# Performance work log

Hardware: AMD Instinct MI355X
Metric: run time of the kernel (lower is better)

Reference implementation:

```python
import jax, jax.numpy as jnp
import numpy as np

B, TQ, TV = 4, 256, 256
H, D, U = 512, 512, 256  # hidden_size, value_size, units


def setup_inputs() -> dict:
    key = jax.random.key(0)
    ks = jax.random.split(key, 8)
    s = 0.02
    return {
        "query": jax.random.normal(ks[0], (B, TQ, H), dtype=jnp.float32),
        "values": jax.random.normal(ks[1], (B, TV, D), dtype=jnp.float32),
        "W1": jax.random.normal(ks[2], (H, U), dtype=jnp.float32) * s,
        "b1": jnp.zeros((U,), dtype=jnp.float32),
        "W2": jax.random.normal(ks[3], (D, U), dtype=jnp.float32) * s,
        "b2": jnp.zeros((U,), dtype=jnp.float32),
        "V": jax.random.normal(ks[4], (U, 1), dtype=jnp.float32) * s,
        "bV": jnp.zeros((1,), dtype=jnp.float32),
    }


def reference(query, values, W1, b1, W2, b2, V, bV):
    # query: [B,Tq,H]  values: [B,Tv,D]
    q = jnp.einsum("bqh,hu->bqu", query, W1) + b1          # [B,Tq,U]
    v = jnp.einsum("bvd,du->bvu", values, W2) + b2          # [B,Tv,U]
    # tf.repeat over Tq is just a broadcast of v; same math without materializing repeats twice
    hidden = jnp.tanh(q[:, :, None, :] + v[:, None, :, :])  # [B,Tq,Tv,U]
    score = jnp.einsum("bqvu,u->bqv", hidden, V[:, 0]) + bV[0]  # [B,Tq,Tv]
    attn = jax.nn.softmax(score, axis=2)                    # softmax over Tv (axis=2 of score)
    context = jnp.einsum("bqv,bvd->bqd", attn, values)      # [B,Tq,D]
    return context, attn[..., None]                          # weights returned as [B,Tq,Tv,1] like TF
```

## Files before the change

### kernel.cpp

```cpp
#include <hip/hip_runtime.h>
#include <math.h>


typedef float f4 __attribute__((ext_vector_type(4)));
typedef float f2 __attribute__((ext_vector_type(2)));
typedef __attribute__((ext_vector_type(8))) short s8v;
typedef __attribute__((ext_vector_type(4))) unsigned short u4v;
typedef __attribute__((ext_vector_type(8))) unsigned short u8v;

#define B_    4
#define TQ_   256
#define TV_   256
#define D_    512
#define U_    256
#define KDIM  512
#define MROWS 1024

#define C2LOG2E 2.8853900817779268f

#define EVT_U16_OFF   524288
#define ATTN_U16_OFF  786432
#define VALT_U16_OFF 1048576

#if __has_builtin(__builtin_amdgcn_exp2f)
#define EXP2F(x) __builtin_amdgcn_exp2f(x)
#else
#define EXP2F(x) exp2f(x)
#endif
#if __has_builtin(__builtin_amdgcn_rcpf)
#define RCPF(x) __builtin_amdgcn_rcpf(x)
#else
#define RCPF(x) (1.0f / (x))
#endif

__device__ __forceinline__ unsigned short f2bf(float f) {
    union { float f; unsigned u; } v; v.f = f;
    return (unsigned short)((v.u + 0x7FFF + ((v.u >> 16) & 1)) >> 16);
}
__device__ __forceinline__ float bf2f(unsigned short h) {
    union { unsigned u; float f; } v; v.u = (unsigned)h << 16;
    return v.f;
}

__global__ __launch_bounds__(256) void proj_mfma(
    const float* __restrict__ query, const float* __restrict__ values,
    const float* __restrict__ W1, const float* __restrict__ b1,
    const float* __restrict__ W2, const float* __restrict__ b2,
    float* __restrict__ ws)
{
    const int tid = threadIdx.x;
    const int job = blockIdx.y;

    if (job == 2) {
        const int idx = blockIdx.x * 256 + tid;
        const int d   = idx & 511;
        const int vg  = (idx >> 9) & 31;
        const int b   = idx >> 14;
        const float* src = values + ((size_t)b * TV_ + vg * 8) * KDIM + d;
        unsigned short* valT = (unsigned short*)ws + VALT_U16_OFF;
        u8v o;
        #pragma unroll
        for (int j = 0; j < 8; ++j) o[j] = f2bf(src[(size_t)j * KDIM]);
        *(u8v*)(valT + ((size_t)b * D_ + d) * TV_ + vg * 8) = o;
        return;
    }

    __shared__ unsigned short Al[2][32][40];
    __shared__ unsigned short Bl[2][32][40];

    const int proj = job;
    const int x    = blockIdx.x;

    int m0, n0;
    if (proj == 0) { m0 = (x >> 3) * 32; n0 = (x & 7) * 32; }
    else           { m0 = (x & 7) * 32;  n0 = (x >> 3) * 32; }

    const int drow = tid >> 3;
    const int dk   = (tid & 7) * 4;
    const int tcol = drow;
    const int tk   = dk;

    const float* dptr = (proj ? values + (size_t)(n0 + drow) * KDIM
                              : query  + (size_t)(m0 + drow) * KDIM) + dk;
    const float* tptr = (proj ? W2 + (m0 + tcol) : W1 + (n0 + tcol))
                        + (size_t)tk * U_;

    f4 d0;
    float tv0, tv1, tv2, tv3;

#define LOADR(S)                                                        \
    do {                                                                \
        d0 = *(const f4*)(dptr + (size_t)(S) * 32);                     \
        const float* tp = tptr + (size_t)(S) * 32 * U_;                 \
        tv0 = tp[0]; tv1 = tp[U_]; tv2 = tp[2 * U_]; tv3 = tp[3 * U_];  \
    } while (0)

#define WRITEB(BUF)                                                     \
    do {                                                                \
        u4v dd, tt;                                                     \
        dd[0] = f2bf(d0[0]); dd[1] = f2bf(d0[1]);                       \
        dd[2] = f2bf(d0[2]); dd[3] = f2bf(d0[3]);                       \
        tt[0] = f2bf(tv0);   tt[1] = f2bf(tv1);                         \
        tt[2] = f2bf(tv2);   tt[3] = f2bf(tv3);                         \
        unsigned short* ddst = proj ? &Bl[BUF][drow][dk] : &Al[BUF][drow][dk]; \
        unsigned short* tdst = proj ? &Al[BUF][tcol][tk] : &Bl[BUF][tcol][tk]; \
        *(u4v*)ddst = dd;                                               \
        *(u4v*)tdst = tt;                                               \
    } while (0)

    f4 acc = {};

    const int w    = tid >> 6;
    const int l    = tid & 63;
    const int fr   = l & 15;
    const int fk   = (l >> 4) * 8;
    const int band = (w & 1) * 16;
    const int colh = (w >> 1) * 16;

    LOADR(0);
    WRITEB(0);

    for (int s = 0; s < 16; ++s) {
        __syncthreads();
        if (s + 1 < 16) LOADR(s + 1);
        {
            const int bu = s & 1;
            s8v af = *(const s8v*)&Al[bu][band + fr][fk];
            s8v bf = *(const s8v*)&Bl[bu][colh + fr][fk];
            acc = __builtin_amdgcn_mfma_f32_16x16x32_bf16(af, bf, acc, 0, 0, 0);
        }
        if (s + 1 < 16) WRITEB((s + 1) & 1);
    }
#undef LOADR
#undef WRITEB

    const int orow = m0 + band + (l >> 4) * 4;
    const int ocol = n0 + colh + (l & 15);

    if (proj == 0) {
        float* E = ws;
        const float bias = b1[ocol];
        #pragma unroll
        for (int r = 0; r < 4; ++r)
            E[(size_t)(orow + r) * U_ + ocol] =
                EXP2F((acc[r] + bias) * C2LOG2E);
    } else {
        unsigned short* E = (unsigned short*)ws + EVT_U16_OFF;
        #pragma unroll
        for (int r = 0; r < 4; ++r)
            E[(size_t)(orow + r) * MROWS + ocol] =
                f2bf(EXP2F((acc[r] + b2[orow + r]) * C2LOG2E));
    }
}

__global__ __launch_bounds__(256) void score_softmax(
    const float* __restrict__ Vw, float* __restrict__ ws,
    float* __restrict__ out)
{
    __shared__ float redmin[4][2];
    __shared__ float redsum[4][2];

    const int tid = threadIdx.x;
    const int b  = blockIdx.y;
    const int q0 = blockIdx.x * 2;

    const float* eq0 = ws + (size_t)(b * TQ_ + q0) * U_;
    const float* eq1 = eq0 + U_;
    const unsigned short* evp =
        (const unsigned short*)ws + EVT_U16_OFF + (size_t)b * TV_ + tid;
    float* attn = out + (size_t)B_ * TQ_ * D_ + (size_t)(b * TQ_ + q0) * TV_;
    unsigned short* attnbf =
        (unsigned short*)ws + ATTN_U16_OFF + (size_t)(b * TQ_ + q0) * TV_;

    float evA[8], evB[8];
    #pragma unroll
    for (int i = 0; i < 8; ++i) evA[i] = bf2f(evp[(size_t)i * MROWS]);

    f2 p = {0.f, 0.f};
    const f2 one = {1.0f, 1.0f};

#define SGRP(BUF, G)                                                    \
    _Pragma("unroll")                                                   \
    for (int i = 0; i < 8; ++i) {                                       \
        const int u = (G) * 8 + i;                                      \
        f2 eq = {eq0[u], eq1[u]};                      \
        f2 ev2 = {BUF[i], BUF[i]};                                      \
        f2 den = eq * ev2 + one;                      \
        f2 r = {RCPF(den.x), RCPF(den.y)};                              \
        f2 wv = {Vw[u], Vw[u]};                             \
        p = wv * r + p;                               \
    }

    #pragma unroll
    for (int g = 0; g < 32; g += 2) {
        #pragma unroll
        for (int i = 0; i < 8; ++i)
            evB[i] = bf2f(evp[(size_t)((g + 1) * 8 + i) * MROWS]);
        SGRP(evA, g)
        if (g + 2 < 32) {
            #pragma unroll
            for (int i = 0; i < 8; ++i)
                evA[i] = bf2f(evp[(size_t)((g + 2) * 8 + i) * MROWS]);
        }
        SGRP(evB, g + 1)
    }
#undef SGRP

    const int w = tid >> 6, lane = tid & 63;
    float m0 = p.x, m1 = p.y;
    #pragma unroll
    for (int off = 32; off; off >>= 1) {
        m0 = fminf(m0, __shfl_xor(m0, off));
        m1 = fminf(m1, __shfl_xor(m1, off));
    }
    if (lane == 0) { redmin[w][0] = m0; redmin[w][1] = m1; }
    __syncthreads();
    m0 = fminf(fminf(redmin[0][0], redmin[1][0]),
               fminf(redmin[2][0], redmin[3][0]));
    m1 = fminf(fminf(redmin[0][1], redmin[1][1]),
               fminf(redmin[2][1], redmin[3][1]));

    float e0 = EXP2F((m0 - p.x) * C2LOG2E);
    float e1 = EXP2F((m1 - p.y) * C2LOG2E);

    float s0 = e0, s1 = e1;
    #pragma unroll
    for (int off = 32; off; off >>= 1) {
        s0 += __shfl_xor(s0, off);
        s1 += __shfl_xor(s1, off);
    }
    if (lane == 0) { redsum[w][0] = s0; redsum[w][1] = s1; }
    __syncthreads();
    s0 = redsum[0][0] + redsum[1][0] + redsum[2][0] + redsum[3][0];
    s1 = redsum[0][1] + redsum[1][1] + redsum[2][1] + redsum[3][1];

    const float a0 = e0 * (1.0f / s0);
    const float a1 = e1 * (1.0f / s1);
    attn[tid]        = a0;
    attn[TV_ + tid]  = a1;
    attnbf[tid]        = f2bf(a0);
    attnbf[TV_ + tid]  = f2bf(a1);
}

__global__ __launch_bounds__(256) void ctx_mfma(
    const float* __restrict__ ws_ro, float* __restrict__ out)
{
    __shared__ unsigned short Al[2][32][72];
    __shared__ unsigned short Bl[2][32][72];

    const int tid = threadIdx.x;
    const int b   = blockIdx.y;
    const int x   = blockIdx.x;
    const int m0  = (x >> 4) * 32;
    const int n0  = (x & 15) * 32;

    const int row  = tid >> 3;
    const int koff = (tid & 7) * 8;

    const unsigned short* attnbf =
        (const unsigned short*)ws_ro + ATTN_U16_OFF;
    const unsigned short* valT =
        (const unsigned short*)ws_ro + VALT_U16_OFF;

    const unsigned short* asrc =
        attnbf + ((size_t)(b * TQ_ + m0 + row)) * TV_ + koff;
    const unsigned short* bsrc =
        valT + ((size_t)(b * D_ + n0 + row)) * TV_ + koff;

    u8v a8, b8;

#define LOADC(S)                                                        \
    do {                                                                \
        a8 = *(const u8v*)(asrc + (S) * 64);                            \
        b8 = *(const u8v*)(bsrc + (S) * 64);                            \
    } while (0)

#define WRITEC(BUF)                                                     \
    do {                                                                \
        *(u8v*)&Al[BUF][row][koff] = a8;                                \
        *(u8v*)&Bl[BUF][row][koff] = b8;                                \
    } while (0)

    f4 acc = {};

    const int w    = tid >> 6;
    const int l    = tid & 63;
    const int fr   = l & 15;
    const int fk   = (l >> 4) * 8;
    const int band = (w & 1) * 16;
    const int colh = (w >> 1) * 16;

    LOADC(0);
    WRITEC(0);

    for (int s = 0; s < 4; ++s) {
        __syncthreads();
        if (s + 1 < 4) LOADC(s + 1);
        {
            const int bu = s & 1;
            s8v af0 = *(const s8v*)&Al[bu][band + fr][fk];
            s8v af1 = *(const s8v*)&Al[bu][band + fr][fk + 32];
            s8v bf0 = *(const s8v*)&Bl[bu][colh + fr][fk];
            s8v bf1 = *(const s8v*)&Bl[bu][colh + fr][fk + 32];
            acc = __builtin_amdgcn_mfma_f32_16x16x32_bf16(af0, bf0, acc, 0, 0, 0);
            acc = __builtin_amdgcn_mfma_f32_16x16x32_bf16(af1, bf1, acc, 0, 0, 0);
        }
        if (s + 1 < 4) WRITEC((s + 1) & 1);
    }
#undef LOADC
#undef WRITEC

    const int orow = m0 + band + (l >> 4) * 4;
    const int ocol = n0 + colh + (l & 15);
    float* C = out + (size_t)b * TQ_ * D_;

    #pragma unroll
    for (int r = 0; r < 4; ++r)
        C[(size_t)(orow + r) * D_ + ocol] = acc[r];
}

extern "C" void kernel_launch(void* const* d_in, const int* in_sizes, int n_in,
                              void* d_out, int out_size, void* d_ws, size_t ws_size,
                              hipStream_t stream) {
    const float* query  = (const float*)d_in[0];
    const float* values = (const float*)d_in[1];
    const float* W1     = (const float*)d_in[2];
    const float* b1     = (const float*)d_in[3];
    const float* W2     = (const float*)d_in[4];
    const float* b2     = (const float*)d_in[5];
    const float* Vw     = (const float*)d_in[6];
    float* out = (float*)d_out;
    float* ws  = (float*)d_ws;

    proj_mfma<<<dim3(256, 3), 256, 0, stream>>>(query, values, W1, b1, W2, b2, ws);
    score_softmax<<<dim3(TQ_ / 2, B_), 256, 0, stream>>>(Vw, ws, out);
    ctx_mfma<<<dim3(128, B_), 256, 0, stream>>>(ws, out);
}
```

Measured before the change: 38.79 us.

## Stage full K panel in LDS once with XOR swizzle, drop per-step sync loop

The projection GEMM used to stream 32-wide K slices through a double-buffered LDS tile, with a barrier every step. It now loads the whole 32x512 A and B panels into registers in one batch, converts them to bf16, and writes them to LDS with an XOR swizzle on 16-byte chunks to avoid bank conflicts. After a single barrier, 16 unrolled MFMAs run with no further synchronization. This removes per-step barriers and exposes many outstanding loads at once, at the cost of much higher register pressure (80 floats of staging) and larger LDS use, which may reduce occupancy.

```diff
diff --git a/kernel.cpp b/kernel.cpp
--- a/kernel.cpp
+++ b/kernel.cpp
@@ -5,7 +5,6 @@
 typedef float f4 __attribute__((ext_vector_type(4)));
 typedef float f2 __attribute__((ext_vector_type(2)));
 typedef __attribute__((ext_vector_type(8))) short s8v;
-typedef __attribute__((ext_vector_type(4))) unsigned short u4v;
 typedef __attribute__((ext_vector_type(8))) unsigned short u8v;
 
 #define B_    4
@@ -41,6 +40,12 @@
     union { unsigned u; float f; } v; v.u = (unsigned)h << 16;
     return v.f;
 }
+__device__ __forceinline__ u8v pack8(const f4 a, const f4 b) {
+    u8v o;
+    o[0] = f2bf(a[0]); o[1] = f2bf(a[1]); o[2] = f2bf(a[2]); o[3] = f2bf(a[3]);
+    o[4] = f2bf(b[0]); o[5] = f2bf(b[1]); o[6] = f2bf(b[2]); o[7] = f2bf(b[3]);
+    return o;
+}
 
 __global__ __launch_bounds__(256) void proj_mfma(
     const float* __restrict__ query, const float* __restrict__ values,
@@ -65,8 +70,8 @@
         return;
     }
 
-    __shared__ unsigned short Al[2][32][40];
-    __shared__ unsigned short Bl[2][32][40];
+    __shared__ u8v Al[32][64];
+    __shared__ u8v Bl[32][64];
 
     const int proj = job;
     const int x    = blockIdx.x;
@@ -76,63 +81,53 @@
     else           { m0 = (x & 7) * 32;  n0 = (x >> 3) * 32; }
 
     const int drow = tid >> 3;
-    const int dk   = (tid & 7) * 4;
-    const int tcol = drow;
-    const int tk   = dk;
-
-    const float* dptr = (proj ? values + (size_t)(n0 + drow) * KDIM
-                              : query  + (size_t)(m0 + drow) * KDIM) + dk;
-    const float* tptr = (proj ? W2 + (m0 + tcol) : W1 + (n0 + tcol))
-                        + (size_t)tk * U_;
-
-    f4 d0;
-    float tv0, tv1, tv2, tv3;
-
-#define LOADR(S)                                                        \
-    do {                                                                \
-        d0 = *(const f4*)(dptr + (size_t)(S) * 32);                     \
-        const float* tp = tptr + (size_t)(S) * 32 * U_;                 \
-        tv0 = tp[0]; tv1 = tp[U_]; tv2 = tp[2 * U_]; tv3 = tp[3 * U_];  \
-    } while (0)
-
-#define WRITEB(BUF)                                                     \
-    do {                                                                \
-        u4v dd, tt;                                                     \
-        dd[0] = f2bf(d0[0]); dd[1] = f2bf(d0[1]);                       \
-        dd[2] = f2bf(d0[2]); dd[3] = f2bf(d0[3]);                       \
-        tt[0] = f2bf(tv0);   tt[1] = f2bf(tv1);                         \
-        tt[2] = f2bf(tv2);   tt[3] = f2bf(tv3);                         \
-        unsigned short* ddst = proj ? &Bl[BUF][drow][dk] : &Al[BUF][drow][dk]; \
-        unsigned short* tdst = proj ? &Al[BUF][tcol][tk] : &Bl[BUF][tcol][tk]; \
-        *(u4v*)ddst = dd;                                               \
-        *(u4v*)tdst = tt;                                               \
-    } while (0)
+    const int duc  = (tid & 7) * 8;
+    const float* dsrc = (proj ? values + (size_t)(n0 + drow) * KDIM
+                              : query  + (size_t)(m0 + drow) * KDIM) + duc * 8;
+
+    const int gcol = tid & 31;
+    const int gk0  = (tid >> 5) * 64;
+    const float* gsrc = (proj ? W2 + (m0 + gcol) : W1 + (n0 + gcol))
+                        + (size_t)gk0 * U_;
+
+    u8v (*DIR)[64] = proj ? Bl : Al;
+    u8v (*GAT)[64] = proj ? Al : Bl;
+
+    f4 dv[16];
+    #pragma unroll
+    for (int j = 0; j < 16; ++j) dv[j] = *(const f4*)(dsrc + j * 4);
+    float gv[64];
+    #pragma unroll
+    for (int j = 0; j < 64; ++j) gv[j] = gsrc[(size_t)j * U_];
+
+    #pragma unroll
+    for (int j = 0; j < 8; ++j)
+        DIR[drow][(duc + j) ^ (drow & 7)] = pack8(dv[2 * j], dv[2 * j + 1]);
+    #pragma unroll
+    for (int g = 0; g < 8; ++g) {
+        u8v o;
+        #pragma unroll
+        for (int j = 0; j < 8; ++j) o[j] = f2bf(gv[g * 8 + j]);
+        GAT[gcol][((gk0 >> 3) + g) ^ (gcol & 7)] = o;
+    }
+    __syncthreads();
 
     f4 acc = {};
-
     const int w    = tid >> 6;
     const int l    = tid & 63;
     const int fr   = l & 15;
-    const int fk   = (l >> 4) * 8;
+    const int fko  = l >> 4;
     const int band = (w & 1) * 16;
     const int colh = (w >> 1) * 16;
-
-    LOADR(0);
-    WRITEB(0);
-
+    const int ar   = band + fr;
+    const int br   = colh + fr;
+
+    #pragma unroll
     for (int s = 0; s < 16; ++s) {
-        __syncthreads();
-        if (s + 1 < 16) LOADR(s + 1);
-        {
-            const int bu = s & 1;
-            s8v af = *(const s8v*)&Al[bu][band + fr][fk];
-            s8v bf = *(const s8v*)&Bl[bu][colh + fr][fk];
-            acc = __builtin_amdgcn_mfma_f32_16x16x32_bf16(af, bf, acc, 0, 0, 0);
-        }
-        if (s + 1 < 16) WRITEB((s + 1) & 1);
-    }
-#undef LOADR
-#undef WRITEB
+        s8v af = *(const s8v*)&Al[ar][(fko + 4 * s) ^ (ar & 7)];
+        s8v bf = *(const s8v*)&Bl[br][(fko + 4 * s) ^ (br & 7)];
+        acc = __builtin_amdgcn_mfma_f32_16x16x32_bf16(af, bf, acc, 0, 0, 0);
+    }
 
     const int orow = m0 + band + (l >> 4) * 4;
     const int ocol = n0 + colh + (l & 15);
```

New measurement: 36.72 us. 5.3% less time.
